# Kernel optimization log

Measured on AMD Instinct MI355X. Metric: run time of the kernel, lower is better.

## Reference

```python
import jax, jax.numpy as jnp
import numpy as np

B, C, H, W = 8, 512, 64, 64
KD, OD = 64, 512

def setup_inputs() -> dict:
    key = jax.random.key(0)
    ks = jax.random.split(key, 8)
    s = 0.05
    return {
        "x":     jax.random.normal(ks[0], (B, C, H, W), dtype=jnp.float32),
        "q_w":   jax.random.normal(ks[1], (KD, C), dtype=jnp.float32) * s,
        "q_b":   jax.random.normal(ks[2], (KD,), dtype=jnp.float32) * s,
        "k_w":   jax.random.normal(ks[3], (KD, C), dtype=jnp.float32) * s,
        "k_b":   jax.random.normal(ks[4], (KD,), dtype=jnp.float32) * s,
        "v_w":   jax.random.normal(ks[5], (OD, C), dtype=jnp.float32) * s,
        "v_b":   jax.random.normal(ks[6], (OD,), dtype=jnp.float32) * s,
        "gamma": jax.random.normal(ks[7], (1,), dtype=jnp.float32) * s,
    }

def reference(x, q_w, q_b, k_w, k_b, v_w, v_b, gamma):
    b, c, h, w = x.shape
    n = h * w
    xf = x.reshape(b, c, n)                                   # [B, C, N]
    # 1x1 convs == per-position matmuls
    q = jnp.einsum('kc,bcn->bkn', q_w, xf) + q_b[:, None]     # [B, KD, N]
    k = jnp.einsum('kc,bcn->bkn', k_w, xf) + k_b[:, None]     # [B, KD, N]
    v = jnp.einsum('oc,bcn->bon', v_w, xf) + v_b[:, None]     # [B, OD, N]
    # energy[b, i, j] = <q[:, i], k[:, j]>  (query permuted to [B, N, KD])
    energy = jnp.einsum('bki,bkj->bij', q, k)                 # [B, N, N]
    attn = jax.nn.softmax(energy, axis=-1)                    # softmax over j
    # out = V @ attn^T : out[b, o, i] = sum_j v[b, o, j] * attn[b, i, j]
    out = jnp.einsum('boj,bij->boi', v, attn)                 # [B, OD, N]
    out = gamma[0] * out + v
    return out.reshape(b, -1, h, w)
```

## Files before the change

kernel.cpp:

```cpp
#include <hip/hip_runtime.h>
#include <hip/hip_bf16.h>

#define BATCH 8
#define CDIM  512
#define NPOS  4096
#define KDQK  64
#define ODIM  512

typedef __attribute__((ext_vector_type(8)))  short short8v;
typedef __attribute__((ext_vector_type(16))) float f32x16;

static __device__ __forceinline__ unsigned short f2bf(float f) {
    union { __hip_bfloat16 h; unsigned short u; } cv;
    cv.h = __float2bfloat16(f);
    return cv.u;
}
static __device__ __forceinline__ float bf2f(unsigned short u) {
    union { unsigned short u; __hip_bfloat16 h; } cv;
    cv.u = u;
    return __bfloat162float(cv.h);
}

static __device__ __forceinline__ void gload_lds16(const unsigned short* g, unsigned short* s) {
    __builtin_amdgcn_global_load_lds((const __attribute__((address_space(1))) unsigned int*)g,
                                     (__attribute__((address_space(3))) unsigned int*)s, 16, 0, 0);
}

static __device__ __forceinline__ int cvtpk(float a, float b) {
    int r;
    asm("v_cvt_pk_bf16_f32 %0, %1, %2" : "=v"(r) : "v"(a), "v"(b));
    return r;
}
static __device__ __forceinline__ void plswap(int& a, int& b) {
    asm("v_permlane32_swap_b32 %0, %1" : "+v"(a), "+v"(b));
}
static __device__ __forceinline__ short8v pack_frag(int a, int b, int c, int d) {
    union { int i[4]; short8v v; } u;
    u.i[0] = a; u.i[1] = b; u.i[2] = c; u.i[3] = d;
    return u.v;
}

__global__ __launch_bounds__(256) void wconv_kernel(const float* __restrict__ qw,
                                                    const float* __restrict__ kw,
                                                    const float* __restrict__ vw,
                                                    unsigned short* __restrict__ wq,
                                                    unsigned short* __restrict__ wk,
                                                    unsigned short* __restrict__ wv) {
    int idx = blockIdx.x * 256 + threadIdx.x;
    if (idx < 32768)        wq[idx]          = f2bf(qw[idx]);
    else if (idx < 65536)   wk[idx - 32768]  = f2bf(kw[idx - 32768]);
    else if (idx < 327680)  wv[idx - 65536]  = f2bf(vw[idx - 65536]);
}

__global__ __launch_bounds__(256) void xpose_kernel(const float* __restrict__ x,
                                                    unsigned short* __restrict__ xT) {
    __shared__ float xs[64][65];
    const int b = blockIdx.z, c0 = blockIdx.y * 64, n0 = blockIdx.x * 64;
    const int t = threadIdx.x;
    #pragma unroll
    for (int it = 0; it < 4; ++it) {
        int lin = it * 256 + t;
        int c = lin >> 4, nq = lin & 15;
        const float4 v = *reinterpret_cast<const float4*>(
            x + ((size_t)(b * CDIM + c0 + c) * NPOS + n0 + nq * 4));
        xs[c][nq * 4 + 0] = v.x; xs[c][nq * 4 + 1] = v.y;
        xs[c][nq * 4 + 2] = v.z; xs[c][nq * 4 + 3] = v.w;
    }
    __syncthreads();
    #pragma unroll
    for (int it = 0; it < 4; ++it) {
        int lin = it * 256 + t;
        int n = lin >> 4, cq = lin & 15;
        ushort4 u;
        u.x = f2bf(xs[cq * 4 + 0][n]); u.y = f2bf(xs[cq * 4 + 1][n]);
        u.z = f2bf(xs[cq * 4 + 2][n]); u.w = f2bf(xs[cq * 4 + 3][n]);
        *reinterpret_cast<ushort4*>(xT + ((size_t)(b * NPOS + n0 + n) * CDIM + c0 + cq * 4)) = u;
    }
}

template <int TRANS>
__global__ __launch_bounds__(256) void proj_kernel(const unsigned short* __restrict__ W,
                                                   const float* __restrict__ bias,
                                                   const unsigned short* __restrict__ xT,
                                                   unsigned short* __restrict__ Y,
                                                   float scale) {
    __shared__ unsigned short Wl[64][64];
    __shared__ unsigned short Xl[64][64];
    const int b = blockIdx.z, r0 = blockIdx.y * 64, n0 = blockIdx.x * 64;
    const int t = threadIdx.x, wave = t >> 6, lane = t & 63, hi = lane >> 5, lo = lane & 31;
    const int wr = wave >> 1, wc = wave & 1;

    f32x16 acc;
    #pragma unroll
    for (int q = 0; q < 16; ++q) acc[q] = 0.f;

    for (int ck = 0; ck < CDIM; ck += 64) {
        __syncthreads();
        #pragma unroll
        for (int it = 0; it < 2; ++it) {
            int lin = it * 256 + t;
            int r = lin >> 3, c8 = lin & 7;
            int4 v = *reinterpret_cast<const int4*>(W + ((size_t)(r0 + r) * CDIM + ck + c8 * 8));
            *reinterpret_cast<int4*>(&Wl[r][(c8 ^ (r & 7)) * 8]) = v;
        }
        #pragma unroll
        for (int it = 0; it < 2; ++it) {
            int lin = it * 256 + t;
            int n = lin >> 3, c8 = lin & 7;
            int4 v = *reinterpret_cast<const int4*>(
                xT + ((size_t)(b * NPOS + n0 + n) * CDIM + ck + c8 * 8));
            *reinterpret_cast<int4*>(&Xl[n][(c8 ^ (n & 7)) * 8]) = v;
        }
        __syncthreads();
        const int ar = wr * 32 + lo, bn = wc * 32 + lo;
        #pragma unroll
        for (int ks = 0; ks < 4; ++ks) {
            int chunk = 2 * ks + hi;
            short8v a  = *reinterpret_cast<const short8v*>(&Wl[ar][(chunk ^ (ar & 7)) * 8]);
            short8v bb = *reinterpret_cast<const short8v*>(&Xl[bn][(chunk ^ (bn & 7)) * 8]);
            acc = __builtin_amdgcn_mfma_f32_32x32x16_bf16(a, bb, acc, 0, 0, 0);
        }
    }

    const int n = n0 + wc * 32 + lo;
    if (TRANS) {
        #pragma unroll
        for (int g = 0; g < 4; ++g) {
            int rbase = wr * 32 + g * 8 + hi * 4;
            ushort4 u;
            u.x = f2bf((acc[4 * g + 0] + bias[r0 + rbase + 0]) * scale);
            u.y = f2bf((acc[4 * g + 1] + bias[r0 + rbase + 1]) * scale);
            u.z = f2bf((acc[4 * g + 2] + bias[r0 + rbase + 2]) * scale);
            u.w = f2bf((acc[4 * g + 3] + bias[r0 + rbase + 3]) * scale);
            *reinterpret_cast<ushort4*>(Y + ((size_t)(b * NPOS + n) * KDQK + r0 + rbase)) = u;
        }
    } else {
        #pragma unroll
        for (int q = 0; q < 16; ++q) {
            int r = r0 + wr * 32 + (q & 3) + 8 * (q >> 2) + 4 * hi;
            Y[(size_t)(b * ODIM + r) * NPOS + n] = f2bf((acc[q] + bias[r]) * scale);
        }
    }
}

__global__ __launch_bounds__(256, 2) void attn_kernel(const unsigned short* __restrict__ Qt,
                                                      const unsigned short* __restrict__ Kt,
                                                      const unsigned short* __restrict__ V,
                                                      const float* __restrict__ gamma_p,
                                                      float* __restrict__ out) {
    __shared__ __align__(16) unsigned short Kbuf[2][32 * 64];
    __shared__ __align__(16) unsigned short Vbuf[2][256 * 32];

    const int bid = blockIdx.x;
    const int pr = bid & 15, b = pr >> 1, oh = pr & 1, qt = bid >> 4;
    const int i0 = qt * 128, od_blk = oh * 256;
    const int tid = threadIdx.x, w = tid >> 6, l = tid & 63;
    const int lo = l & 31, hi = l >> 5;
    const int qg = w >> 1, oq = w & 1;
    const int iw0 = i0 + qg * 64;
    const int ow0 = od_blk + oq * 128;
    const int kswz = lo & 7, vswz = (lo >> 1) & 3;

    const int krow = w * 8 + (l >> 3);
    const unsigned short* kp = Kt + ((size_t)b * NPOS + krow) * KDQK + (((l & 7) ^ (krow & 7)) << 3);
    const unsigned short* vp[4];
    #pragma unroll
    for (int v = 0; v < 4; ++v) {
        int vrow = (w * 4 + v) * 16 + (l >> 2);
        vp[v] = V + ((size_t)b * ODIM + od_blk + vrow) * NPOS + (((l & 3) ^ ((vrow >> 1) & 3)) << 3);
    }

    short8v qf0[4], qf1[4];
    #pragma unroll
    for (int ks = 0; ks < 4; ++ks) {
        qf0[ks] = *reinterpret_cast<const short8v*>(
            Qt + ((size_t)b * NPOS + iw0 + lo) * KDQK + (2 * ks + hi) * 8);
        qf1[ks] = *reinterpret_cast<const short8v*>(
            Qt + ((size_t)b * NPOS + iw0 + 32 + lo) * KDQK + (2 * ks + hi) * 8);
    }

    f32x16 acc[4][2];
    #pragma unroll
    for (int mt = 0; mt < 4; ++mt)
        #pragma unroll
        for (int q = 0; q < 16; ++q) { acc[mt][0][q] = 0.f; acc[mt][1][q] = 0.f; }

    float m0 = -1e30f, m1 = -1e30f, lsum0 = 0.f, lsum1 = 0.f;

    gload_lds16(kp, &Kbuf[0][w * 512]);
    #pragma unroll
    for (int v = 0; v < 4; ++v) gload_lds16(vp[v], &Vbuf[0][(w * 4 + v) * 512]);
    kp += 32 * KDQK;
    #pragma unroll
    for (int v = 0; v < 4; ++v) vp[v] += 32;
    __syncthreads();

    int cur = 0;
    for (int jt = 0; jt < NPOS / 32; ++jt) {
        if (jt < NPOS / 32 - 1) {
            int nb = cur ^ 1;
            gload_lds16(kp, &Kbuf[nb][w * 512]);
            #pragma unroll
            for (int v = 0; v < 4; ++v) gload_lds16(vp[v], &Vbuf[nb][(w * 4 + v) * 512]);
            kp += 32 * KDQK;
            #pragma unroll
            for (int v = 0; v < 4; ++v) vp[v] += 32;
        }
        const unsigned short* KB = Kbuf[cur];
        const unsigned short* VB = Vbuf[cur];

        f32x16 s0, s1;
        #pragma unroll
        for (int q = 0; q < 16; ++q) { s0[q] = 0.f; s1[q] = 0.f; }
        __builtin_amdgcn_s_setprio(1);
        #pragma unroll
        for (int ks = 0; ks < 4; ++ks) {
            short8v a = *reinterpret_cast<const short8v*>(
                KB + lo * 64 + (((2 * ks + hi) ^ kswz) << 3));
            s0 = __builtin_amdgcn_mfma_f32_32x32x16_bf16(a, qf0[ks], s0, 0, 0, 0);
            s1 = __builtin_amdgcn_mfma_f32_32x32x16_bf16(a, qf1[ks], s1, 0, 0, 0);
        }
        __builtin_amdgcn_s_setprio(0);

        float mx0 = s0[0], mx1 = s1[0];
        #pragma unroll
        for (int q = 1; q < 16; ++q) { mx0 = fmaxf(mx0, s0[q]); mx1 = fmaxf(mx1, s1[q]); }
        mx0 = fmaxf(mx0, __shfl_xor(mx0, 32));
        mx1 = fmaxf(mx1, __shfl_xor(mx1, 32));

        bool ok = (mx0 <= m0 + 12.f) && (mx1 <= m1 + 12.f);
        if (!__all(ok)) {
            float mn0 = fmaxf(m0, mx0), mn1 = fmaxf(m1, mx1);
            float c0 = exp2f(m0 - mn0), c1 = exp2f(m1 - mn1);
            m0 = mn0; m1 = mn1; lsum0 *= c0; lsum1 *= c1;
            #pragma unroll
            for (int mt = 0; mt < 4; ++mt)
                #pragma unroll
                for (int q = 0; q < 16; ++q) { acc[mt][0][q] *= c0; acc[mt][1][q] *= c1; }
        }

        float rs0 = 0.f, rs1 = 0.f;
        #pragma unroll
        for (int q = 0; q < 16; ++q) {
            s0[q] = exp2f(s0[q] - m0); rs0 += s0[q];
            s1[q] = exp2f(s1[q] - m1); rs1 += s1[q];
        }
        rs0 += __shfl_xor(rs0, 32);
        rs1 += __shfl_xor(rs1, 32);
        lsum0 += rs0; lsum1 += rs1;

        #pragma unroll
        for (int ks = 0; ks < 2; ++ks) {
            int xa0 = cvtpk(s0[8 * ks + 0], s0[8 * ks + 1]), ya0 = cvtpk(s0[8 * ks + 2], s0[8 * ks + 3]);
            int xb0 = cvtpk(s0[8 * ks + 4], s0[8 * ks + 5]), yb0 = cvtpk(s0[8 * ks + 6], s0[8 * ks + 7]);
            int xa1 = cvtpk(s1[8 * ks + 0], s1[8 * ks + 1]), ya1 = cvtpk(s1[8 * ks + 2], s1[8 * ks + 3]);
            int xb1 = cvtpk(s1[8 * ks + 4], s1[8 * ks + 5]), yb1 = cvtpk(s1[8 * ks + 6], s1[8 * ks + 7]);
            plswap(xa0, xb0); plswap(ya0, yb0);
            plswap(xa1, xb1); plswap(ya1, yb1);
            short8v pb0 = pack_frag(xa0, ya0, xb0, yb0);
            short8v pb1 = pack_frag(xa1, ya1, xb1, yb1);
            __builtin_amdgcn_s_setprio(1);
            #pragma unroll
            for (int mt = 0; mt < 4; ++mt) {
                short8v av = *reinterpret_cast<const short8v*>(
                    VB + (oq * 128 + mt * 32 + lo) * 32 + (((2 * ks + hi) ^ vswz) << 3));
                acc[mt][0] = __builtin_amdgcn_mfma_f32_32x32x16_bf16(av, pb0, acc[mt][0], 0, 0, 0);
                acc[mt][1] = __builtin_amdgcn_mfma_f32_32x32x16_bf16(av, pb1, acc[mt][1], 0, 0, 0);
            }
            __builtin_amdgcn_s_setprio(0);
        }
        __syncthreads();
        cur ^= 1;
    }

    float inv0 = 1.0f / lsum0, inv1 = 1.0f / lsum1;
    const float gm = gamma_p[0];
    #pragma unroll
    for (int mt = 0; mt < 4; ++mt) {
        #pragma unroll
        for (int g = 0; g < 4; ++g) {
            #pragma unroll
            for (int d = 0; d < 4; ++d) {
                int q = 4 * g + d;
                int od = ow0 + mt * 32 + d + 8 * g + 4 * hi;
                size_t base = ((size_t)b * ODIM + od) * NPOS;
                int ia = iw0 + lo, ib = iw0 + 32 + lo;
                out[base + ia] = gm * acc[mt][0][q] * inv0 + bf2f(V[base + ia]);
                out[base + ib] = gm * acc[mt][1][q] * inv1 + bf2f(V[base + ib]);
            }
        }
    }
}

extern "C" void kernel_launch(void* const* d_in, const int* in_sizes, int n_in,
                              void* d_out, int out_size, void* d_ws, size_t ws_size,
                              hipStream_t stream) {
    const float* x     = (const float*)d_in[0];
    const float* qw    = (const float*)d_in[1];
    const float* qb    = (const float*)d_in[2];
    const float* kw    = (const float*)d_in[3];
    const float* kb    = (const float*)d_in[4];
    const float* vw    = (const float*)d_in[5];
    const float* vb    = (const float*)d_in[6];
    const float* gamma = (const float*)d_in[7];
    float* out = (float*)d_out;

    char* ws = (char*)d_ws;
    unsigned short* xT = (unsigned short*)(ws);
    unsigned short* wq = (unsigned short*)(ws + 33554432);
    unsigned short* wk = (unsigned short*)(ws + 33619968);
    unsigned short* wv = (unsigned short*)(ws + 33685504);
    unsigned short* Qt = (unsigned short*)(ws + 34209792);
    unsigned short* Kt = (unsigned short*)(ws + 38404096);
    unsigned short* Vn = (unsigned short*)(ws + 42598400);

    wconv_kernel<<<1280, 256, 0, stream>>>(qw, kw, vw, wq, wk, wv);
    xpose_kernel<<<dim3(64, 8, 8), 256, 0, stream>>>(x, xT);
    proj_kernel<1><<<dim3(64, 1, 8), 256, 0, stream>>>(wq, qb, xT, Qt, 1.44269504f);
    proj_kernel<1><<<dim3(64, 1, 8), 256, 0, stream>>>(wk, kb, xT, Kt, 1.0f);
    proj_kernel<0><<<dim3(64, 8, 8), 256, 0, stream>>>(wv, vb, xT, Vn, 1.0f);
    attn_kernel<<<512, 256, 0, stream>>>(Qt, Kt, Vn, gamma, out);
}
```

Measured before the change: 464.5 us.

## Restructure attention kernel: 512-thread blocks covering all output channels, P shared via LDS

The attention kernel now uses 512-thread blocks that each handle 64 query positions across all 512 output channels, so QK^T and softmax are computed once per query tile instead of twice (previously split across two od halves). Each wave computes scores for a 32x32 slice of a 128-wide key tile. Row max and sum are combined across waves through LDS, and the bf16 probabilities are written to a swizzled LDS buffer that all waves read as MFMA B operands. V is now read directly from global memory instead of being staged in LDS, and exp2 uses the raw hardware builtin. The change adds two block barriers per tile and relies on V global loads being cached.

```diff
diff --git a/kernel.cpp b/kernel.cpp
--- a/kernel.cpp
+++ b/kernel.cpp
@@ -31,14 +31,12 @@
     asm("v_cvt_pk_bf16_f32 %0, %1, %2" : "=v"(r) : "v"(a), "v"(b));
     return r;
 }
-static __device__ __forceinline__ void plswap(int& a, int& b) {
-    asm("v_permlane32_swap_b32 %0, %1" : "+v"(a), "+v"(b));
-}
-static __device__ __forceinline__ short8v pack_frag(int a, int b, int c, int d) {
-    union { int i[4]; short8v v; } u;
-    u.i[0] = a; u.i[1] = b; u.i[2] = c; u.i[3] = d;
-    return u.v;
-}
+
+#if __has_builtin(__builtin_amdgcn_exp2f)
+static __device__ __forceinline__ float exp2_raw(float x) { return __builtin_amdgcn_exp2f(x); }
+#else
+static __device__ __forceinline__ float exp2_raw(float x) { return exp2f(x); }
+#endif
 
 __global__ __launch_bounds__(256) void wconv_kernel(const float* __restrict__ qw,
                                                     const float* __restrict__ kw,
@@ -143,150 +141,156 @@
     }
 }
 
-__global__ __launch_bounds__(256, 2) void attn_kernel(const unsigned short* __restrict__ Qt,
+__global__ __launch_bounds__(512, 2) void attn_kernel(const unsigned short* __restrict__ Qt,
                                                       const unsigned short* __restrict__ Kt,
                                                       const unsigned short* __restrict__ V,
                                                       const float* __restrict__ gamma_p,
                                                       float* __restrict__ out) {
-    __shared__ __align__(16) unsigned short Kbuf[2][32 * 64];
-    __shared__ __align__(16) unsigned short Vbuf[2][256 * 32];
+    __shared__ __align__(16) unsigned short Kbuf[2][128 * 64];
+    __shared__ __align__(16) unsigned short Pl[64 * 128];
+    __shared__ __align__(16) float maxb[64][4];
+    __shared__ __align__(16) float sumb[64][4];
 
     const int bid = blockIdx.x;
-    const int pr = bid & 15, b = pr >> 1, oh = pr & 1, qt = bid >> 4;
-    const int i0 = qt * 128, od_blk = oh * 256;
-    const int tid = threadIdx.x, w = tid >> 6, l = tid & 63;
-    const int lo = l & 31, hi = l >> 5;
-    const int qg = w >> 1, oq = w & 1;
-    const int iw0 = i0 + qg * 64;
-    const int ow0 = od_blk + oq * 128;
-    const int kswz = lo & 7, vswz = (lo >> 1) & 3;
-
-    const int krow = w * 8 + (l >> 3);
-    const unsigned short* kp = Kt + ((size_t)b * NPOS + krow) * KDQK + (((l & 7) ^ (krow & 7)) << 3);
-    const unsigned short* vp[4];
-    #pragma unroll
-    for (int v = 0; v < 4; ++v) {
-        int vrow = (w * 4 + v) * 16 + (l >> 2);
-        vp[v] = V + ((size_t)b * ODIM + od_blk + vrow) * NPOS + (((l & 3) ^ ((vrow >> 1) & 3)) << 3);
-    }
-
-    short8v qf0[4], qf1[4];
-    #pragma unroll
-    for (int ks = 0; ks < 4; ++ks) {
-        qf0[ks] = *reinterpret_cast<const short8v*>(
-            Qt + ((size_t)b * NPOS + iw0 + lo) * KDQK + (2 * ks + hi) * 8);
-        qf1[ks] = *reinterpret_cast<const short8v*>(
-            Qt + ((size_t)b * NPOS + iw0 + 32 + lo) * KDQK + (2 * ks + hi) * 8);
-    }
-
-    f32x16 acc[4][2];
-    #pragma unroll
-    for (int mt = 0; mt < 4; ++mt)
-        #pragma unroll
-        for (int q = 0; q < 16; ++q) { acc[mt][0][q] = 0.f; acc[mt][1][q] = 0.f; }
-
-    float m0 = -1e30f, m1 = -1e30f, lsum0 = 0.f, lsum1 = 0.f;
-
-    gload_lds16(kp, &Kbuf[0][w * 512]);
-    #pragma unroll
-    for (int v = 0; v < 4; ++v) gload_lds16(vp[v], &Vbuf[0][(w * 4 + v) * 512]);
-    kp += 32 * KDQK;
-    #pragma unroll
-    for (int v = 0; v < 4; ++v) vp[v] += 32;
+    const int b = bid & 7, qt = bid >> 3;
+    const int i0 = qt * 64;
+    const int tid = threadIdx.x, wid = tid >> 6, l = tid & 63, lo = l & 31, hi = l >> 5;
+    const int jh = wid >> 1, ih = wid & 1;
+    const int ow0 = wid * 64;
+
+    const int sidx0 = tid, sidx1 = 512 + tid;
+    const int srow0 = sidx0 >> 3, srow1 = sidx1 >> 3;
+    const unsigned short* kp0 = Kt + ((size_t)b * NPOS + srow0) * 64 + (((sidx0 & 7) ^ (srow0 & 7)) << 3);
+    const unsigned short* kp1 = Kt + ((size_t)b * NPOS + srow1) * 64 + (((sidx1 & 7) ^ (srow1 & 7)) << 3);
+    const int kd0 = sidx0 * 8, kd1 = sidx1 * 8;
+
+    short8v qf[4];
+    {
+        const unsigned short* qb = Qt + ((size_t)b * NPOS + i0 + ih * 32 + lo) * 64 + hi * 8;
+        #pragma unroll
+        for (int kc = 0; kc < 4; ++kc)
+            qf[kc] = *reinterpret_cast<const short8v*>(qb + kc * 16);
+    }
+
+    f32x16 acc[2][2];
+    #pragma unroll
+    for (int odt = 0; odt < 2; ++odt)
+        #pragma unroll
+        for (int q = 0; q < 16; ++q) { acc[odt][0][q] = 0.f; acc[odt][1][q] = 0.f; }
+
+    float mr0 = -1e30f, mr1 = -1e30f, lr0 = 0.f, lr1 = 0.f;
+
+    gload_lds16(kp0, &Kbuf[0][kd0]);
+    gload_lds16(kp1, &Kbuf[0][kd1]);
     __syncthreads();
 
-    int cur = 0;
-    for (int jt = 0; jt < NPOS / 32; ++jt) {
-        if (jt < NPOS / 32 - 1) {
-            int nb = cur ^ 1;
-            gload_lds16(kp, &Kbuf[nb][w * 512]);
+    const int krow = jh * 32 + lo;
+    const unsigned short* Vbase = V + ((size_t)b * ODIM + ow0 + lo) * NPOS + hi * 8;
+
+    for (int t = 0; t < 32; ++t) {
+        const int j0 = t * 128;
+        const int bi = t & 1;
+
+        f32x16 s;
+        #pragma unroll
+        for (int q = 0; q < 16; ++q) s[q] = 0.f;
+        const unsigned short* KB = &Kbuf[bi][0];
+        #pragma unroll
+        for (int kc = 0; kc < 4; ++kc) {
+            short8v a = *reinterpret_cast<const short8v*>(
+                KB + krow * 64 + (((kc * 2 + hi) ^ (krow & 7)) << 3));
+            s = __builtin_amdgcn_mfma_f32_32x32x16_bf16(a, qf[kc], s, 0, 0, 0);
+        }
+        float m01 = fmaxf(s[0], s[1]),   m23 = fmaxf(s[2], s[3]);
+        float m45 = fmaxf(s[4], s[5]),   m67 = fmaxf(s[6], s[7]);
+        float m89 = fmaxf(s[8], s[9]),   mab = fmaxf(s[10], s[11]);
+        float mcd = fmaxf(s[12], s[13]), mef = fmaxf(s[14], s[15]);
+        float mx = fmaxf(fmaxf(fmaxf(m01, m23), fmaxf(m45, m67)),
+                         fmaxf(fmaxf(m89, mab), fmaxf(mcd, mef)));
+        mx = fmaxf(mx, __shfl_xor(mx, 32));
+        if (hi == 0) maxb[ih * 32 + lo][jh] = mx;
+        __syncthreads();
+
+        if (t + 1 < 32) {
+            gload_lds16(kp0 + (size_t)(j0 + 128) * 64, &Kbuf[bi ^ 1][kd0]);
+            gload_lds16(kp1 + (size_t)(j0 + 128) * 64, &Kbuf[bi ^ 1][kd1]);
+        }
+        float4 mv0 = *reinterpret_cast<const float4*>(&maxb[lo][0]);
+        float4 mv1 = *reinterpret_cast<const float4*>(&maxb[32 + lo][0]);
+        float mt0 = fmaxf(fmaxf(mv0.x, mv0.y), fmaxf(mv0.z, mv0.w));
+        float mt1 = fmaxf(fmaxf(mv1.x, mv1.y), fmaxf(mv1.z, mv1.w));
+        bool g0 = mt0 > mr0 + 12.f, g1 = mt1 > mr1 + 12.f;
+        float c0 = g0 ? exp2_raw(mr0 - mt0) : 1.f;
+        float c1 = g1 ? exp2_raw(mr1 - mt1) : 1.f;
+        if (g0) mr0 = mt0;
+        if (g1) mr1 = mt1;
+        float msel = ih ? mr1 : mr0;
+
+        float p[16];
+        #pragma unroll
+        for (int q = 0; q < 16; ++q) p[q] = exp2_raw(s[q] - msel);
+        float t01 = (p[0] + p[1]) + (p[2] + p[3]);
+        float t23 = (p[4] + p[5]) + (p[6] + p[7]);
+        float t45 = (p[8] + p[9]) + (p[10] + p[11]);
+        float t67 = (p[12] + p[13]) + (p[14] + p[15]);
+        float ts = (t01 + t23) + (t45 + t67);
+        ts += __shfl_xor(ts, 32);
+        if (hi == 0) sumb[ih * 32 + lo][jh] = ts;
+
+        {
+            const int irow = ih * 32 + lo;
+            const int rk = irow & 15;
             #pragma unroll
-            for (int v = 0; v < 4; ++v) gload_lds16(vp[v], &Vbuf[nb][(w * 4 + v) * 512]);
-            kp += 32 * KDQK;
+            for (int m = 0; m < 4; ++m) {
+                int w0 = cvtpk(p[4 * m + 0], p[4 * m + 1]);
+                int w1 = cvtpk(p[4 * m + 2], p[4 * m + 3]);
+                int pos = (jh * 4 + m) ^ rk;
+                *reinterpret_cast<int2*>(&Pl[irow * 128 + pos * 8 + hi * 4]) = make_int2(w0, w1);
+            }
+        }
+        __syncthreads();
+
+        float4 sv0 = *reinterpret_cast<const float4*>(&sumb[lo][0]);
+        float4 sv1 = *reinterpret_cast<const float4*>(&sumb[32 + lo][0]);
+        float ts0 = (sv0.x + sv0.y) + (sv0.z + sv0.w);
+        float ts1 = (sv1.x + sv1.y) + (sv1.z + sv1.w);
+        lr0 = lr0 * c0 + ts0;
+        lr1 = lr1 * c1 + ts1;
+        if (__any(g0 || g1)) {
             #pragma unroll
-            for (int v = 0; v < 4; ++v) vp[v] += 32;
-        }
-        const unsigned short* KB = Kbuf[cur];
-        const unsigned short* VB = Vbuf[cur];
-
-        f32x16 s0, s1;
-        #pragma unroll
-        for (int q = 0; q < 16; ++q) { s0[q] = 0.f; s1[q] = 0.f; }
-        __builtin_amdgcn_s_setprio(1);
-        #pragma unroll
-        for (int ks = 0; ks < 4; ++ks) {
-            short8v a = *reinterpret_cast<const short8v*>(
-                KB + lo * 64 + (((2 * ks + hi) ^ kswz) << 3));
-            s0 = __builtin_amdgcn_mfma_f32_32x32x16_bf16(a, qf0[ks], s0, 0, 0, 0);
-            s1 = __builtin_amdgcn_mfma_f32_32x32x16_bf16(a, qf1[ks], s1, 0, 0, 0);
-        }
-        __builtin_amdgcn_s_setprio(0);
-
-        float mx0 = s0[0], mx1 = s1[0];
-        #pragma unroll
-        for (int q = 1; q < 16; ++q) { mx0 = fmaxf(mx0, s0[q]); mx1 = fmaxf(mx1, s1[q]); }
-        mx0 = fmaxf(mx0, __shfl_xor(mx0, 32));
-        mx1 = fmaxf(mx1, __shfl_xor(mx1, 32));
-
-        bool ok = (mx0 <= m0 + 12.f) && (mx1 <= m1 + 12.f);
-        if (!__all(ok)) {
-            float mn0 = fmaxf(m0, mx0), mn1 = fmaxf(m1, mx1);
-            float c0 = exp2f(m0 - mn0), c1 = exp2f(m1 - mn1);
-            m0 = mn0; m1 = mn1; lsum0 *= c0; lsum1 *= c1;
+            for (int odt = 0; odt < 2; ++odt)
+                #pragma unroll
+                for (int q = 0; q < 16; ++q) { acc[odt][0][q] *= c0; acc[odt][1][q] *= c1; }
+        }
+        const int rk = lo & 15;
+        #pragma unroll
+        for (int odt = 0; odt < 2; ++odt) {
             #pragma unroll
-            for (int mt = 0; mt < 4; ++mt)
-                #pragma unroll
-                for (int q = 0; q < 16; ++q) { acc[mt][0][q] *= c0; acc[mt][1][q] *= c1; }
-        }
-
-        float rs0 = 0.f, rs1 = 0.f;
-        #pragma unroll
-        for (int q = 0; q < 16; ++q) {
-            s0[q] = exp2f(s0[q] - m0); rs0 += s0[q];
-            s1[q] = exp2f(s1[q] - m1); rs1 += s1[q];
-        }
-        rs0 += __shfl_xor(rs0, 32);
-        rs1 += __shfl_xor(rs1, 32);
-        lsum0 += rs0; lsum1 += rs1;
-
-        #pragma unroll
-        for (int ks = 0; ks < 2; ++ks) {
-            int xa0 = cvtpk(s0[8 * ks + 0], s0[8 * ks + 1]), ya0 = cvtpk(s0[8 * ks + 2], s0[8 * ks + 3]);
-            int xb0 = cvtpk(s0[8 * ks + 4], s0[8 * ks + 5]), yb0 = cvtpk(s0[8 * ks + 6], s0[8 * ks + 7]);
-            int xa1 = cvtpk(s1[8 * ks + 0], s1[8 * ks + 1]), ya1 = cvtpk(s1[8 * ks + 2], s1[8 * ks + 3]);
-            int xb1 = cvtpk(s1[8 * ks + 4], s1[8 * ks + 5]), yb1 = cvtpk(s1[8 * ks + 6], s1[8 * ks + 7]);
-            plswap(xa0, xb0); plswap(ya0, yb0);
-            plswap(xa1, xb1); plswap(ya1, yb1);
-            short8v pb0 = pack_frag(xa0, ya0, xb0, yb0);
-            short8v pb1 = pack_frag(xa1, ya1, xb1, yb1);
-            __builtin_amdgcn_s_setprio(1);
+            for (int kc = 0; kc < 8; ++kc) {
+                short8v av = *reinterpret_cast<const short8v*>(
+                    Vbase + (size_t)odt * 32 * NPOS + j0 + kc * 16);
+                int pos = ((kc * 2 + hi) ^ rk) * 8;
+                short8v b0 = *reinterpret_cast<const short8v*>(&Pl[lo * 128 + pos]);
+                short8v b1 = *reinterpret_cast<const short8v*>(&Pl[(32 + lo) * 128 + pos]);
+                acc[odt][0] = __builtin_amdgcn_mfma_f32_32x32x16_bf16(av, b0, acc[odt][0], 0, 0, 0);
+                acc[odt][1] = __builtin_amdgcn_mfma_f32_32x32x16_bf16(av, b1, acc[odt][1], 0, 0, 0);
+            }
+        }
+    }
+
+    float inv0 = 1.0f / lr0, inv1 = 1.0f / lr1;
+    const float gm = gamma_p[0];
+    #pragma unroll
+    for (int odt = 0; odt < 2; ++odt) {
+        #pragma unroll
+        for (int it = 0; it < 2; ++it) {
+            float inv = it ? inv1 : inv0;
             #pragma unroll
-            for (int mt = 0; mt < 4; ++mt) {
-                short8v av = *reinterpret_cast<const short8v*>(
-                    VB + (oq * 128 + mt * 32 + lo) * 32 + (((2 * ks + hi) ^ vswz) << 3));
-                acc[mt][0] = __builtin_amdgcn_mfma_f32_32x32x16_bf16(av, pb0, acc[mt][0], 0, 0, 0);
-                acc[mt][1] = __builtin_amdgcn_mfma_f32_32x32x16_bf16(av, pb1, acc[mt][1], 0, 0, 0);
-            }
-            __builtin_amdgcn_s_setprio(0);
-        }
-        __syncthreads();
-        cur ^= 1;
-    }
-
-    float inv0 = 1.0f / lsum0, inv1 = 1.0f / lsum1;
-    const float gm = gamma_p[0];
-    #pragma unroll
-    for (int mt = 0; mt < 4; ++mt) {
-        #pragma unroll
-        for (int g = 0; g < 4; ++g) {
-            #pragma unroll
-            for (int d = 0; d < 4; ++d) {
-                int q = 4 * g + d;
-                int od = ow0 + mt * 32 + d + 8 * g + 4 * hi;
-                size_t base = ((size_t)b * ODIM + od) * NPOS;
-                int ia = iw0 + lo, ib = iw0 + 32 + lo;
-                out[base + ia] = gm * acc[mt][0][q] * inv0 + bf2f(V[base + ia]);
-                out[base + ib] = gm * acc[mt][1][q] * inv1 + bf2f(V[base + ib]);
+            for (int q = 0; q < 16; ++q) {
+                int od = ow0 + odt * 32 + (q & 3) + 8 * (q >> 2) + 4 * hi;
+                int i = i0 + it * 32 + lo;
+                size_t addr = ((size_t)b * ODIM + od) * NPOS + i;
+                out[addr] = gm * acc[odt][it][q] * inv + bf2f(V[addr]);
             }
         }
     }
@@ -319,5 +323,5 @@
     proj_kernel<1><<<dim3(64, 1, 8), 256, 0, stream>>>(wq, qb, xT, Qt, 1.44269504f);
     proj_kernel<1><<<dim3(64, 1, 8), 256, 0, stream>>>(wk, kb, xT, Kt, 1.0f);
     proj_kernel<0><<<dim3(64, 8, 8), 256, 0, stream>>>(wv, vb, xT, Vn, 1.0f);
-    attn_kernel<<<512, 256, 0, stream>>>(Qt, Kt, Vn, gamma, out);
-}
+    attn_kernel<<<512, 512, 0, stream>>>(Qt, Kt, Vn, gamma, out);
+}
```

Result: slower. 483.1 us (+4.0%).
